# Optimization experiments

Measured on AMD Instinct MI355X. Metric: run time of the kernel, lower is better.

## Reference

```python
import math
import jax, jax.numpy as jnp
import numpy as np

C, NH, NL, NP, NLAYERS, FFN = 256, 8, 3, 4, 6, 1024
DH = C // NH
SHAPES = ((64, 64), (32, 32), (16, 16))  # (H,W) for res3, res4, res5
SIZES = [h * w for h, w in SHAPES]
STARTS = np.cumsum([0] + SIZES[:-1]).tolist()
EPS = 1e-5


def _sin_pe(H, W):
    d = C // 4
    y = jnp.arange(H, dtype=jnp.float32)[:, None]
    x = jnp.arange(W, dtype=jnp.float32)[None, :]
    div = jnp.exp(jnp.arange(d, dtype=jnp.float32) * (-math.log(10000.0) / d))[:, None, None]
    pe = jnp.concatenate([
        jnp.broadcast_to(jnp.sin(y * div), (d, H, W)),
        jnp.broadcast_to(jnp.cos(y * div), (d, H, W)),
        jnp.broadcast_to(jnp.sin(x * div), (d, H, W)),
        jnp.broadcast_to(jnp.cos(x * div), (d, H, W)),
    ], axis=0)  # (C,H,W)
    return pe.reshape(C, H * W).T  # (HW, C)


def _ref_points():
    pts = []
    for H, W in SHAPES:
        y = jnp.linspace(0.5 / H, 1.0 - 0.5 / H, H)
        x = jnp.linspace(0.5 / W, 1.0 - 0.5 / W, W)
        ry, rx = jnp.meshgrid(y, x, indexing='ij')
        pts.append(jnp.stack([rx.ravel(), ry.ravel()], -1))
    return jnp.concatenate(pts, 0)[None, :, None, :]  # (1,N,1,2), same per level


def _layernorm(x, g, b):
    mu = x.mean(-1, keepdims=True)
    v = ((x - mu) ** 2).mean(-1, keepdims=True)
    return (x - mu) * jax.lax.rsqrt(v + EPS) * g + b


def _bilinear(v, loc, H, W):
    # v: (B,HW,NH,DH); loc: (B,N,NH,NP,2) in [0,1]; grid_sample align_corners=False, zero pad
    B, N = loc.shape[0], loc.shape[1]
    x = loc[..., 0] * W - 0.5
    y = loc[..., 1] * H - 0.5
    x0 = jnp.floor(x); y0 = jnp.floor(y)
    wx = x - x0; wy = y - y0
    x0i = x0.astype(jnp.int32); y0i = y0.astype(jnp.int32)
    v_t = jnp.transpose(v, (0, 2, 1, 3))  # (B,NH,HW,DH)

    def corner(xi, yi, w):
        valid = (xi >= 0) & (xi < W) & (yi >= 0) & (yi < H)
        idx = jnp.clip(yi, 0, H - 1) * W + jnp.clip(xi, 0, W - 1)  # (B,N,NH,NP)
        idx = jnp.transpose(idx, (0, 2, 1, 3)).reshape(B, NH, N * NP)
        g = jnp.take_along_axis(v_t, idx[..., None], axis=2)  # (B,NH,N*NP,DH)
        g = g.reshape(B, NH, N, NP, DH).transpose(0, 2, 1, 3, 4)
        return g * (w * valid)[..., None]

    return (corner(x0i, y0i, (1 - wx) * (1 - wy))
            + corner(x0i + 1, y0i, wx * (1 - wy))
            + corner(x0i, y0i + 1, (1 - wx) * wy)
            + corner(x0i + 1, y0i + 1, wx * wy))


def _forward(res2, res3, res4, res5, level_embed, off_W, off_b, aw_W, aw_b, val_W, val_b,
             out_W, out_b, ln1_g, ln1_b, fc1_W, fc1_b, fc2_W, fc2_b, ln2_g, ln2_b,
             lat_W, lat_b, sm_W, sm_b, gn_g, gn_b):
    feats = [res3, res4, res5]
    B = res3.shape[0]
    flat = jnp.concatenate(
        [f.reshape(B, C, -1).transpose(0, 2, 1) + level_embed[i] for i, f in enumerate(feats)], 1)
    pe = jnp.concatenate([_sin_pe(H, W) for H, W in SHAPES], 0)[None]  # (1,N,C)
    ref = _ref_points()  # (1,N,1,2)
    normalizer = jnp.array([[W, H] for H, W in SHAPES], jnp.float32)  # (NL,2) as (W,H)
    N = flat.shape[1]

    x = flat
    for l in range(NLAYERS):
        q = x + pe
        value = (x @ val_W[l].T + val_b[l]).reshape(B, N, NH, DH)
        off = (q @ off_W[l].T + off_b[l]).reshape(B, N, NH, NL, NP, 2)
        aw = jax.nn.softmax((q @ aw_W[l].T + aw_b[l]).reshape(B, N, NH, NL * NP), -1)
        aw = aw.reshape(B, N, NH, NL, NP)
        loc = ref[:, :, None, :, None, :] + off / normalizer[None, None, None, :, None, :]
        attn = jnp.zeros((B, N, NH, DH), x.dtype)
        for li, (H, W) in enumerate(SHAPES):
            v_l = value[:, STARTS[li]:STARTS[li] + SIZES[li]]
            samp = _bilinear(v_l, loc[:, :, :, li], H, W)  # (B,N,NH,NP,DH)
            attn = attn + jnp.einsum('bnhpd,bnhp->bnhd', samp, aw[:, :, :, li])
        attn = attn.reshape(B, N, C) @ out_W[l].T + out_b[l]
        x = _layernorm(x + attn, ln1_g[l], ln1_b[l])
        h = jax.nn.relu(x @ fc1_W[l].T + fc1_b[l]) @ fc2_W[l].T + fc2_b[l]
        x = _layernorm(x + h, ln2_g[l], ln2_b[l])

    outs = []
    for li, (H, W) in enumerate(SHAPES):
        tok = x[:, STARTS[li]:STARTS[li] + SIZES[li]]
        outs.append(tok.transpose(0, 2, 1).reshape(B, C, H, W))
    o3, o4, o5 = outs

    r2_lat = jnp.einsum('bchw,oc->bohw', res2, lat_W) + lat_b[None, :, None, None]
    Hr, Wr = res2.shape[2], res2.shape[3]
    r3_up = jax.image.resize(o3, (B, C, Hr, Wr), method='bilinear')
    s = jax.lax.conv_general_dilated(r2_lat + r3_up, sm_W, (1, 1), ((1, 1), (1, 1)),
                                     dimension_numbers=('NCHW', 'OIHW', 'NCHW'))
    s = s + sm_b[None, :, None, None]
    # GroupNorm(32, C)
    g = s.reshape(B, 32, C // 32, Hr, Wr)
    mu = g.mean((2, 3, 4), keepdims=True)
    var = jnp.var(g, axis=(2, 3, 4), keepdims=True)
    g = (g - mu) * jax.lax.rsqrt(var + EPS)
    s = g.reshape(B, C, Hr, Wr) * gn_g[None, :, None, None] + gn_b[None, :, None, None]
    s = jax.nn.gelu(s, approximate=False)
    return s, o3, o4, o5


def setup_inputs() -> dict:
    key = jax.random.key(0)
    ks = jax.random.split(key, 16)
    def rn(k, shape, s=0.02):
        return jax.random.normal(k, shape, jnp.float32) * s
    B = 2
    L = NLAYERS
    return {
        'res2': jax.random.normal(ks[0], (B, C, 128, 128), jnp.float32),
        'res3': jax.random.normal(ks[1], (B, C, 64, 64), jnp.float32),
        'res4': jax.random.normal(ks[2], (B, C, 32, 32), jnp.float32),
        'res5': jax.random.normal(ks[3], (B, C, 16, 16), jnp.float32),
        'level_embed': rn(ks[4], (NL, C)),
        'off_W': rn(ks[5], (L, NH * NL * NP * 2, C)), 'off_b': jnp.zeros((L, NH * NL * NP * 2)),
        'aw_W': rn(ks[6], (L, NH * NL * NP, C)), 'aw_b': jnp.zeros((L, NH * NL * NP)),
        'val_W': rn(ks[7], (L, C, C)), 'val_b': jnp.zeros((L, C)),
        'out_W': rn(ks[8], (L, C, C)), 'out_b': jnp.zeros((L, C)),
        'ln1_g': jnp.ones((L, C)), 'ln1_b': jnp.zeros((L, C)),
        'fc1_W': rn(ks[9], (L, FFN, C)), 'fc1_b': jnp.zeros((L, FFN)),
        'fc2_W': rn(ks[10], (L, C, FFN)), 'fc2_b': jnp.zeros((L, C)),
        'ln2_g': jnp.ones((L, C)), 'ln2_b': jnp.zeros((L, C)),
        'lat_W': rn(ks[11], (C, C)), 'lat_b': jnp.zeros((C,)),
        'sm_W': rn(ks[12], (C, C, 3, 3)), 'sm_b': jnp.zeros((C,)),
        'gn_g': jnp.ones((C,)), 'gn_b': jnp.zeros((C,)),
    }


def reference(res2, res3, res4, res5, level_embed, off_W, off_b, aw_W, aw_b, val_W, val_b,
              out_W, out_b, ln1_g, ln1_b, fc1_W, fc1_b, fc2_W, fc2_b, ln2_g, ln2_b,
              lat_W, lat_b, sm_W, sm_b, gn_g, gn_b):
    return _forward(res2, res3, res4, res5, level_embed, off_W, off_b, aw_W, aw_b,
                    val_W, val_b, out_W, out_b, ln1_g, ln1_b, fc1_W, fc1_b, fc2_W, fc2_b,
                    ln2_g, ln2_b, lat_W, lat_b, sm_W, sm_b, gn_g, gn_b)
```

## Files before the change

### kernel.cpp

```cpp
#include <hip/hip_runtime.h>

namespace {
constexpr int Bn   = 2;
constexpr int Cc   = 256;
constexpr int Ntok = 5376;
constexpr int Ffn  = 1024;
constexpr int HW2  = 128 * 128;
constexpr float EPSf = 1e-5f;
constexpr int WL   = 729088;
}

typedef __attribute__((ext_vector_type(8))) short bf16x8;
typedef __attribute__((ext_vector_type(4))) float f32x4;

__device__ inline unsigned short f2bf(float x) {
  unsigned u = __float_as_uint(x);
  return (unsigned short)((u + 0x7fffu + ((u >> 16) & 1u)) >> 16);
}
__device__ inline float bf2f(unsigned short b) {
  return __uint_as_float((unsigned)b << 16);
}

__device__ inline void store_chunk_f32(unsigned short* lds, int row, int g,
                                       const float* v8) {
  int sg = g ^ (row & 7);
  unsigned short tmp[8];
#pragma unroll
  for (int j = 0; j < 8; j++) tmp[j] = f2bf(v8[j]);
  *reinterpret_cast<uint4*>(&lds[row * 64 + sg * 8]) =
      *reinterpret_cast<const uint4*>(tmp);
}
__device__ inline void store_chunk_bf(unsigned short* lds, int row, int g,
                                      uint4 v) {
  int sg = g ^ (row & 7);
  *reinterpret_cast<uint4*>(&lds[row * 64 + sg * 8]) = v;
}

__global__ __launch_bounds__(256) void wprep(
    const float* __restrict__ valW, const float* __restrict__ offW,
    const float* __restrict__ awW, const float* __restrict__ outW,
    const float* __restrict__ fc1W, const float* __restrict__ fc2W,
    const float* __restrict__ latW, const float* __restrict__ smW,
    unsigned short* __restrict__ wbf, unsigned short* __restrict__ wlat,
    unsigned short* __restrict__ wt) {
  int bx = blockIdx.x;
  int tid = threadIdx.x;
  if (bx < 4272) {
    int i4 = bx * 256 + tid;
    int l = i4 / 182272;
    int e = (i4 - l * 182272) * 4;
    const float* src;
    int off;
    if (e < 65536) { src = valW + (size_t)l * 65536; off = e; }
    else if (e < 139264) {
      int j = e - 65536;
      if (j < 49152) { src = offW + (size_t)l * 49152; off = j; }
      else { src = awW + (size_t)l * 24576; off = j - 49152; }
    } else if (e < 204800) { src = outW + (size_t)l * 65536; off = e - 139264; }
    else if (e < 466944) { src = fc1W + (size_t)l * 262144; off = e - 204800; }
    else { src = fc2W + (size_t)l * 262144; off = e - 466944; }
    float4 v = *reinterpret_cast<const float4*>(&src[off]);
    unsigned short t[4] = {f2bf(v.x), f2bf(v.y), f2bf(v.z), f2bf(v.w)};
    *reinterpret_cast<uint2*>(&wbf[(size_t)l * WL + e]) =
        *reinterpret_cast<const uint2*>(t);
  } else if (bx < 4336) {
    int e = ((bx - 4272) * 256 + tid) * 4;
    float4 v = *reinterpret_cast<const float4*>(&latW[e]);
    unsigned short t[4] = {f2bf(v.x), f2bf(v.y), f2bf(v.z), f2bf(v.w)};
    *reinterpret_cast<uint2*>(&wlat[e]) = *reinterpret_cast<const uint2*>(t);
  } else {
    int i = (bx - 4336) * 256 + tid;
    int o = i / 2304;
    int r = i - o * 2304;
    int tap = r >> 8;
    int c = r & 255;
    wt[i] = f2bf(smW[((size_t)(o * 256 + c)) * 9 + tap]);
  }
}

__global__ void flatten_kernel(const float* __restrict__ r3,
                               const float* __restrict__ r4,
                               const float* __restrict__ r5,
                               const float* __restrict__ lemb,
                               float* __restrict__ x,
                               unsigned short* __restrict__ xb,
                               unsigned short* __restrict__ qb,
                               unsigned short* __restrict__ peb) {
  const int NPC = Ntok * Cc;
  for (int i = blockIdx.x * blockDim.x + threadIdx.x; i < Bn * NPC;
       i += gridDim.x * blockDim.x) {
    int c = i & 255;
    int rest = i >> 8;
    int p = rest % Ntok;
    int b = rest / Ntok;
    int li = (p < 4096) ? 0 : ((p < 5120) ? 1 : 2);
    int start = (li == 0) ? 0 : ((li == 1) ? 4096 : 5120);
    int size = (li == 0) ? 4096 : ((li == 1) ? 1024 : 256);
    const float* f = (li == 0) ? r3 : ((li == 1) ? r4 : r5);
    int sp = p - start;
    int shift = 6 - li;
    int W = 64 >> li;
    int iy = sp >> shift;
    int ix = sp & (W - 1);
    int j = c & 63;
    int sel = c >> 6;
    float div = expf(-(float)j * (9.210340371976184f / 64.f));
    float coord = (sel < 2) ? (float)iy : (float)ix;
    float arg = coord * div;
    unsigned short pe16 = f2bf((sel & 1) ? cosf(arg) : sinf(arg));
    float v = f[((size_t)(b * Cc + c)) * size + sp] + lemb[li * Cc + c];
    x[i] = v;
    xb[i] = f2bf(v);
    qb[i] = f2bf(v + bf2f(pe16));
    peb[i - b * NPC] = pe16;
  }
}

template <int ACT, int OBF>
__global__ __launch_bounds__(256) void gemm_mfma_b(
    const unsigned short* __restrict__ A, const unsigned short* __restrict__ Wb,
    const float* __restrict__ bias, void* __restrict__ outp,
    int M, int N, int K, int nbx) {
  __shared__ unsigned short As[64 * 64];
  __shared__ unsigned short Ws[128 * 64];
  const int tid = threadIdx.x;
  const int nwg = gridDim.x;
  const int swz = (blockIdx.x & 7) * (nwg >> 3) + (blockIdx.x >> 3);
  const int m0 = (swz / nbx) * 64, n0 = (swz % nbx) * 128;
  const int wid = tid >> 6, lane = tid & 63;
  const int wm = wid >> 1, wn = wid & 1;
  const int lr = lane & 15, lh = lane >> 4;
  const int r8 = tid >> 3, g8 = tid & 7;
  f32x4 acc[2][4];
#pragma unroll
  for (int i = 0; i < 2; i++)
#pragma unroll
    for (int j = 0; j < 4; j++) acc[i][j] = f32x4{0.f, 0.f, 0.f, 0.f};

  uint4 ra[2], rw[4];
  const uint4 z4 = uint4{0, 0, 0, 0};
#pragma unroll
  for (int i = 0; i < 2; i++)
    ra[i] = *reinterpret_cast<const uint4*>(
        &A[(size_t)(m0 + r8 + i * 32) * K + g8 * 8]);
#pragma unroll
  for (int i = 0; i < 4; i++) {
    int n = n0 + r8 + i * 32;
    rw[i] = (n < N) ? *reinterpret_cast<const uint4*>(
                          &Wb[(size_t)n * K + g8 * 8])
                    : z4;
  }

  for (int k0 = 0; k0 < K; k0 += 64) {
    if (k0) __syncthreads();
#pragma unroll
    for (int i = 0; i < 2; i++) store_chunk_bf(As, r8 + i * 32, g8, ra[i]);
#pragma unroll
    for (int i = 0; i < 4; i++) store_chunk_bf(Ws, r8 + i * 32, g8, rw[i]);
    __syncthreads();
    int kn = k0 + 64;
    if (kn < K) {
#pragma unroll
      for (int i = 0; i < 2; i++)
        ra[i] = *reinterpret_cast<const uint4*>(
            &A[(size_t)(m0 + r8 + i * 32) * K + kn + g8 * 8]);
#pragma unroll
      for (int i = 0; i < 4; i++) {
        int n = n0 + r8 + i * 32;
        rw[i] = (n < N) ? *reinterpret_cast<const uint4*>(
                              &Wb[(size_t)n * K + kn + g8 * 8])
                        : z4;
      }
    }
    bf16x8 af[2][2], bfr[4][2];
#pragma unroll
    for (int mi = 0; mi < 2; mi++) {
      int r = wm * 32 + mi * 16 + lr;
#pragma unroll
      for (int s = 0; s < 2; s++) {
        int g = s * 4 + lh;
        af[mi][s] =
            *reinterpret_cast<const bf16x8*>(&As[r * 64 + (g ^ (r & 7)) * 8]);
      }
    }
#pragma unroll
    for (int nj = 0; nj < 4; nj++) {
      int r = wn * 64 + nj * 16 + lr;
#pragma unroll
      for (int s = 0; s < 2; s++) {
        int g = s * 4 + lh;
        bfr[nj][s] =
            *reinterpret_cast<const bf16x8*>(&Ws[r * 64 + (g ^ (r & 7)) * 8]);
      }
    }
#pragma unroll
    for (int mi = 0; mi < 2; mi++)
#pragma unroll
      for (int nj = 0; nj < 4; nj++) {
        acc[mi][nj] = __builtin_amdgcn_mfma_f32_16x16x32_bf16(
            af[mi][0], bfr[nj][0], acc[mi][nj], 0, 0, 0);
        acc[mi][nj] = __builtin_amdgcn_mfma_f32_16x16x32_bf16(
            af[mi][1], bfr[nj][1], acc[mi][nj], 0, 0, 0);
      }
  }
#pragma unroll
  for (int mi = 0; mi < 2; mi++) {
    int row = m0 + wm * 32 + mi * 16 + lh * 4;
#pragma unroll
    for (int nj = 0; nj < 4; nj++) {
      int col = n0 + wn * 64 + nj * 16 + lr;
      if (col >= N) continue;
      float b = bias[col];
#pragma unroll
      for (int r = 0; r < 4; r++) {
        float v = acc[mi][nj][r] + b;
        if (ACT) v = fmaxf(v, 0.f);
        if (OBF)
          ((unsigned short*)outp)[(size_t)(row + r) * N + col] = f2bf(v);
        else
          ((float*)outp)[(size_t)(row + r) * N + col] = v;
      }
    }
  }
}

template <int WRITEQ, int TOKOUT>
__global__ __launch_bounds__(256) void gemm_ln(
    const unsigned short* __restrict__ A, const unsigned short* __restrict__ Wb,
    const float* __restrict__ bias, const float* __restrict__ g,
    const float* __restrict__ bta, float* __restrict__ x,
    unsigned short* __restrict__ xb, const unsigned short* __restrict__ peb,
    unsigned short* __restrict__ qb, int K, float* __restrict__ o3,
    float* __restrict__ o4, float* __restrict__ o5) {
  __shared__ unsigned short As[32 * 64];
  __shared__ unsigned short Ws[256 * 64];
  __shared__ float pred[2][2][16];
  __shared__ float qred[2][2][16];
  const int tid = threadIdx.x;
  const int swz = (blockIdx.x & 7) * 42 + (blockIdx.x >> 3);
  const int m0 = swz * 32;
  const int wid = tid >> 6, lane = tid & 63;
  const int wm = wid >> 1, wn = wid & 1;
  const int lr = lane & 15, lh = lane >> 4;
  const int r8 = tid >> 3, g8 = tid & 7;
  f32x4 acc[8];
#pragma unroll
  for (int i = 0; i < 8; i++) acc[i] = f32x4{0.f, 0.f, 0.f, 0.f};

  uint4 ra, rw[8];
  ra = *reinterpret_cast<const uint4*>(&A[(size_t)(m0 + r8) * K + g8 * 8]);
#pragma unroll
  for (int i = 0; i < 8; i++)
    rw[i] = *reinterpret_cast<const uint4*>(
        &Wb[(size_t)(r8 + i * 32) * K + g8 * 8]);

  for (int k0 = 0; k0 < K; k0 += 64) {
    if (k0) __syncthreads();
    store_chunk_bf(As, r8, g8, ra);
#pragma unroll
    for (int i = 0; i < 8; i++) store_chunk_bf(Ws, r8 + i * 32, g8, rw[i]);
    __syncthreads();
    int kn = k0 + 64;
    if (kn < K) {
      ra = *reinterpret_cast<const uint4*>(
          &A[(size_t)(m0 + r8) * K + kn + g8 * 8]);
#pragma unroll
      for (int i = 0; i < 8; i++)
        rw[i] = *reinterpret_cast<const uint4*>(
            &Wb[(size_t)(r8 + i * 32) * K + kn + g8 * 8]);
    }
    bf16x8 af[2];
    {
      int r = wm * 16 + lr;
#pragma unroll
      for (int s = 0; s < 2; s++) {
        int gg2 = s * 4 + lh;
        af[s] =
            *reinterpret_cast<const bf16x8*>(&As[r * 64 + (gg2 ^ (r & 7)) * 8]);
      }
    }
#pragma unroll
    for (int nt = 0; nt < 8; nt++) {
      int r = wn * 128 + nt * 16 + lr;
      bf16x8 b0 =
          *reinterpret_cast<const bf16x8*>(&Ws[r * 64 + (lh ^ (r & 7)) * 8]);
      bf16x8 b1 = *reinterpret_cast<const bf16x8*>(
          &Ws[r * 64 + ((4 + lh) ^ (r & 7)) * 8]);
      acc[nt] =
          __builtin_amdgcn_mfma_f32_16x16x32_bf16(af[0], b0, acc[nt], 0, 0, 0);
      acc[nt] =
          __builtin_amdgcn_mfma_f32_16x16x32_bf16(af[1], b1, acc[nt], 0, 0, 0);
    }
  }

  const int rowl = wm * 16 + lh * 4;
#pragma unroll
  for (int nt = 0; nt < 8; nt++) {
    int col = wn * 128 + nt * 16 + lr;
    float bs = bias[col];
#pragma unroll
    for (int r = 0; r < 4; r++)
      acc[nt][r] += bs + x[(size_t)(m0 + rowl + r) * 256 + col];
  }
  float sum[4];
#pragma unroll
  for (int r = 0; r < 4; r++) {
    float s = 0.f;
#pragma unroll
    for (int nt = 0; nt < 8; nt++) s += acc[nt][r];
#pragma unroll
    for (int o = 8; o > 0; o >>= 1) s += __shfl_xor(s, o);
    sum[r] = s;
  }
  if (lr == 0) {
#pragma unroll
    for (int r = 0; r < 4; r++) pred[wm][wn][lh * 4 + r] = sum[r];
  }
  __syncthreads();
  float mu[4];
#pragma unroll
  for (int r = 0; r < 4; r++)
    mu[r] = (pred[wm][0][lh * 4 + r] + pred[wm][1][lh * 4 + r]) * (1.f / 256.f);
  float qs[4];
#pragma unroll
  for (int r = 0; r < 4; r++) {
    float q = 0.f;
#pragma unroll
    for (int nt = 0; nt < 8; nt++) {
      float d = acc[nt][r] - mu[r];
      q += d * d;
    }
#pragma unroll
    for (int o = 8; o > 0; o >>= 1) q += __shfl_xor(q, o);
    qs[r] = q;
  }
  if (lr == 0) {
#pragma unroll
    for (int r = 0; r < 4; r++) qred[wm][wn][lh * 4 + r] = qs[r];
  }
  __syncthreads();
  float rstd[4];
#pragma unroll
  for (int r = 0; r < 4; r++)
    rstd[r] = rsqrtf(
        (qred[wm][0][lh * 4 + r] + qred[wm][1][lh * 4 + r]) * (1.f / 256.f) +
        EPSf);
  float oarr[8][4];
#pragma unroll
  for (int nt = 0; nt < 8; nt++) {
    int col = wn * 128 + nt * 16 + lr;
    float gw = g[col], bw = bta[col];
#pragma unroll
    for (int r = 0; r < 4; r++) {
      int row = m0 + rowl + r;
      size_t idx = (size_t)row * 256 + col;
      float o = (acc[nt][r] - mu[r]) * rstd[r] * gw + bw;
      x[idx] = o;
      xb[idx] = f2bf(o);
      if (WRITEQ) {
        size_t pc = idx - (row >= Ntok ? (size_t)Ntok * 256 : 0);
        qb[idx] = f2bf(o + bf2f(peb[pc]));
      }
      if (TOKOUT) oarr[nt][r] = o;
    }
  }
  if constexpr (TOKOUT) {
    __shared__ float tout[32][129];
    int bb = (m0 >= Ntok) ? 1 : 0;
    int n = m0 - bb * Ntok;
    float* outp;
    int osize, ostart;
    if (n < 4096) { outp = o3; osize = 4096; ostart = 0; }
    else if (n < 5120) { outp = o4; osize = 1024; ostart = 4096; }
    else { outp = o5; osize = 256; ostart = 5120; }
    int sp0 = n - ostart;
#pragma unroll
    for (int hh = 0; hh < 2; hh++) {
      __syncthreads();
      if (wn == hh) {
#pragma unroll
        for (int nt = 0; nt < 8; nt++) {
          int cl = nt * 16 + lr;
#pragma unroll
          for (int r = 0; r < 4; r++) tout[rowl + r][cl] = oarr[nt][r];
        }
      }
      __syncthreads();
      int cl = tid & 127, rh = tid >> 7;
      float* dst =
          outp + ((size_t)(bb * 256 + hh * 128 + cl)) * osize + sp0 + rh * 16;
#pragma unroll
      for (int i = 0; i < 16; i += 4) {
        float4 v4 = {tout[rh * 16 + i + 0][cl], tout[rh * 16 + i + 1][cl],
                     tout[rh * 16 + i + 2][cl], tout[rh * 16 + i + 3][cl]};
        *reinterpret_cast<float4*>(&dst[i]) = v4;
      }
    }
  }
}

__global__ __launch_bounds__(256) void gemm_head(
    const unsigned short* __restrict__ xb, const unsigned short* __restrict__ qb,
    const unsigned short* __restrict__ wv, const unsigned short* __restrict__ wo,
    const float* __restrict__ valB, const float* __restrict__ offB,
    const float* __restrict__ awB, unsigned short* __restrict__ valO,
    float* __restrict__ offO, float* __restrict__ awO) {
  __shared__ unsigned short As[64 * 64];
  __shared__ unsigned short Ws[128 * 64];
  const int tid = threadIdx.x;
  const int swz = (blockIdx.x & 7) * 105 + (blockIdx.x >> 3);
  const bool isval = swz < 336;
  const unsigned short* A;
  const unsigned short* W;
  int m0, n0, Nn;
  if (isval) {
    A = xb; W = wv; Nn = 256;
    m0 = (swz >> 1) * 64; n0 = (swz & 1) * 128;
  } else {
    int s = swz - 336;
    A = qb; W = wo; Nn = 288;
    m0 = (s / 3) * 64; n0 = (s % 3) * 128;
  }
  const int wid = tid >> 6, lane = tid & 63;
  const int wm = wid >> 1, wn = wid & 1;
  const int lr = lane & 15, lh = lane >> 4;
  const int r8 = tid >> 3, g8 = tid & 7;
  f32x4 acc[2][4];
#pragma unroll
  for (int i = 0; i < 2; i++)
#pragma unroll
    for (int j = 0; j < 4; j++) acc[i][j] = f32x4{0.f, 0.f, 0.f, 0.f};

  uint4 ra[2], rw[4];
  const uint4 z4 = uint4{0, 0, 0, 0};
#pragma unroll
  for (int i = 0; i < 2; i++)
    ra[i] = *reinterpret_cast<const uint4*>(
        &A[(size_t)(m0 + r8 + i * 32) * 256 + g8 * 8]);
#pragma unroll
  for (int i = 0; i < 4; i++) {
    int n = n0 + r8 + i * 32;
    rw[i] = (n < Nn) ? *reinterpret_cast<const uint4*>(
                           &W[(size_t)n * 256 + g8 * 8])
                     : z4;
  }

  for (int k0 = 0; k0 < 256; k0 += 64) {
    if (k0) __syncthreads();
#pragma unroll
    for (int i = 0; i < 2; i++) store_chunk_bf(As, r8 + i * 32, g8, ra[i]);
#pragma unroll
    for (int i = 0; i < 4; i++) store_chunk_bf(Ws, r8 + i * 32, g8, rw[i]);
    __syncthreads();
    int kn = k0 + 64;
    if (kn < 256) {
#pragma unroll
      for (int i = 0; i < 2; i++)
        ra[i] = *reinterpret_cast<const uint4*>(
            &A[(size_t)(m0 + r8 + i * 32) * 256 + kn + g8 * 8]);
#pragma unroll
      for (int i = 0; i < 4; i++) {
        int n = n0 + r8 + i * 32;
        rw[i] = (n < Nn) ? *reinterpret_cast<const uint4*>(
                               &W[(size_t)n * 256 + kn + g8 * 8])
                         : z4;
      }
    }
    bf16x8 af[2][2], bfr[4][2];
#pragma unroll
    for (int mi = 0; mi < 2; mi++) {
      int r = wm * 32 + mi * 16 + lr;
#pragma unroll
      for (int s = 0; s < 2; s++) {
        int g = s * 4 + lh;
        af[mi][s] =
            *reinterpret_cast<const bf16x8*>(&As[r * 64 + (g ^ (r & 7)) * 8]);
      }
    }
#pragma unroll
    for (int nj = 0; nj < 4; nj++) {
      int r = wn * 64 + nj * 16 + lr;
#pragma unroll
      for (int s = 0; s < 2; s++) {
        int g = s * 4 + lh;
        bfr[nj][s] =
            *reinterpret_cast<const bf16x8*>(&Ws[r * 64 + (g ^ (r & 7)) * 8]);
      }
    }
#pragma unroll
    for (int mi = 0; mi < 2; mi++)
#pragma unroll
      for (int nj = 0; nj < 4; nj++) {
        acc[mi][nj] = __builtin_amdgcn_mfma_f32_16x16x32_bf16(
            af[mi][0], bfr[nj][0], acc[mi][nj], 0, 0, 0);
        acc[mi][nj] = __builtin_amdgcn_mfma_f32_16x16x32_bf16(
            af[mi][1], bfr[nj][1], acc[mi][nj], 0, 0, 0);
      }
  }
#pragma unroll
  for (int mi = 0; mi < 2; mi++) {
    int row = m0 + wm * 32 + mi * 16 + lh * 4;
#pragma unroll
    for (int nj = 0; nj < 4; nj++) {
      int col = n0 + wn * 64 + nj * 16 + lr;
      if (isval) {
        float b = valB[col];
#pragma unroll
        for (int r = 0; r < 4; r++)
          valO[(size_t)(row + r) * 256 + col] = f2bf(acc[mi][nj][r] + b);
      } else {
        if (col >= 288) continue;
        float b = (col < 192) ? offB[col] : awB[col - 192];
#pragma unroll
        for (int r = 0; r < 4; r++) {
          float v = acc[mi][nj][r] + b;
          if (col < 192)
            offO[(size_t)(row + r) * 192 + col] = v;
          else
            awO[(size_t)(row + r) * 96 + col - 192] = v;
        }
      }
    }
  }
}

__global__ __launch_bounds__(256) void msda_fused(
    const unsigned short* __restrict__ value, const float* __restrict__ off,
    const float* __restrict__ awl, unsigned short* __restrict__ attn) {
  __shared__ int recI[8][12][4];
  __shared__ float recW[8][12][4];
  const int tid = threadIdx.x;
  if (tid < 96) {
    int gq = tid / 12;
    int p = tid - gq * 12;
    int gid = blockIdx.x * 8 + gq;
    int h = gid & 7;
    int bn = gid >> 3;
    int n = bn % Ntok;
    int b = bn / Ntok;
    int li0 = (n < 4096) ? 0 : ((n < 5120) ? 1 : 2);
    int start0 = (li0 == 0) ? 0 : ((li0 == 1) ? 4096 : 5120);
    int shift = 6 - li0;
    int Wn = 1 << shift;
    int sp = n - start0;
    int iy = sp >> shift;
    int ix = sp & (Wn - 1);
    float refx = (ix + 0.5f) / (float)Wn;
    float refy = (iy + 0.5f) / (float)Wn;
    const float* ap = awl + (size_t)bn * 96 + h * 12;
    float lg[12];
    float mx = -1e30f;
#pragma unroll
    for (int j = 0; j < 12; j++) { lg[j] = ap[j]; mx = fmaxf(mx, lg[j]); }
    float ssum = 0.f;
#pragma unroll
    for (int j = 0; j < 12; j++) { lg[j] = expf(lg[j] - mx); ssum += lg[j]; }
    float w = lg[p] / ssum;
    int li = p >> 2;
    int HWl = 64 >> li;
    int st = (li == 0) ? 0 : ((li == 1) ? 4096 : 5120);
    const float* op = off + (size_t)bn * 192 + h * 24;
    float ox = op[p * 2 + 0];
    float oy = op[p * 2 + 1];
    float lx = refx + ox / (float)HWl;
    float ly = refy + oy / (float)HWl;
    float fx = lx * (float)HWl - 0.5f;
    float fy = ly * (float)HWl - 0.5f;
    float x0f = floorf(fx), y0f = floorf(fy);
    float wx = fx - x0f, wy = fy - y0f;
    int ix0 = (int)x0f, iy0 = (int)y0f;
    int base = (b * Ntok + st) * 256 + h * 32;
#pragma unroll
    for (int cr = 0; cr < 4; cr++) {
      int cx = ix0 + (cr & 1);
      int cy = iy0 + (cr >> 1);
      bool valid = (cx >= 0) & (cx < HWl) & (cy >= 0) & (cy < HWl);
      float wc = ((cr & 1) ? wx : 1.f - wx) * ((cr >> 1) ? wy : 1.f - wy);
      int cxc = min(max(cx, 0), HWl - 1);
      int cyc = min(max(cy, 0), HWl - 1);
      recI[gq][p][cr] = base + (cyc * HWl + cxc) * 256;
      recW[gq][p][cr] = valid ? (w * wc) : 0.f;
    }
  }
  __syncthreads();
  const int grp = tid >> 5, lane = tid & 31;
  const unsigned short* vb = value + lane;
  float acc = 0.f;
#pragma unroll
  for (int p = 0; p < 12; p++) {
    int4 idx = *reinterpret_cast<const int4*>(&recI[grp][p][0]);
    float4 w = *reinterpret_cast<const float4*>(&recW[grp][p][0]);
    acc += w.x * bf2f(vb[idx.x]);
    acc += w.y * bf2f(vb[idx.y]);
    acc += w.z * bf2f(vb[idx.z]);
    acc += w.w * bf2f(vb[idx.w]);
  }
  int gid = blockIdx.x * 8 + grp;
  attn[(size_t)gid * 32 + lane] = f2bf(acc);
}

__global__ __launch_bounds__(256) void conv3x3_mfma(
    const unsigned short* __restrict__ T, const unsigned short* __restrict__ Wt,
    const float* __restrict__ bias, unsigned short* __restrict__ out) {
  __shared__ unsigned short As[64 * 64];
  __shared__ unsigned short Ws[128 * 64];
  const int tid = threadIdx.x;
  const int nwg = gridDim.x;
  const int swz = (blockIdx.x & 7) * (nwg >> 3) + (blockIdx.x >> 3);
  const int m0 = (swz >> 1) * 64, n0 = (swz & 1) * 128;
  const int b = m0 >> 14;
  const int p0 = m0 & 16383;
  const int y = p0 >> 7;
  const int x0 = p0 & 127;
  const int wid = tid >> 6, lane = tid & 63;
  const int wm = wid >> 1, wn = wid & 1;
  const int lr = lane & 15, lh = lane >> 4;
  const int r8 = tid >> 3, g8 = tid & 7;
  f32x4 acc[2][4];
#pragma unroll
  for (int i = 0; i < 2; i++)
#pragma unroll
    for (int j = 0; j < 4; j++) acc[i][j] = f32x4{0.f, 0.f, 0.f, 0.f};

  uint4 ra[2], rw[4];
  auto loadA = [&](int kc, uint4* r) {
    int tap = kc >> 2;
    int cb = (kc & 3) * 64;
    int dy = tap / 3 - 1, dx = tap % 3 - 1;
    int yy = y + dy;
#pragma unroll
    for (int i = 0; i < 2; i++) {
      int row = r8 + i * 32;
      int xx = x0 + row + dx;
      uint4 v = uint4{0, 0, 0, 0};
      if (yy >= 0 && yy < 128 && xx >= 0 && xx < 128)
        v = *reinterpret_cast<const uint4*>(
            &T[((size_t)(b * 16384 + yy * 128 + xx)) * 256 + cb + g8 * 8]);
      r[i] = v;
    }
  };
  auto loadW = [&](int kc, uint4* r) {
#pragma unroll
    for (int i = 0; i < 4; i++)
      r[i] = *reinterpret_cast<const uint4*>(
          &Wt[(size_t)(n0 + r8 + i * 32) * 2304 + kc * 64 + g8 * 8]);
  };
  loadA(0, ra);
  loadW(0, rw);

  for (int kc = 0; kc < 36; kc++) {
    if (kc) __syncthreads();
#pragma unroll
    for (int i = 0; i < 2; i++) store_chunk_bf(As, r8 + i * 32, g8, ra[i]);
#pragma unroll
    for (int i = 0; i < 4; i++) store_chunk_bf(Ws, r8 + i * 32, g8, rw[i]);
    __syncthreads();
    if (kc + 1 < 36) {
      loadA(kc + 1, ra);
      loadW(kc + 1, rw);
    }
    bf16x8 af[2][2], bfr[4][2];
#pragma unroll
    for (int mi = 0; mi < 2; mi++) {
      int r = wm * 32 + mi * 16 + lr;
#pragma unroll
      for (int s = 0; s < 2; s++) {
        int g = s * 4 + lh;
        af[mi][s] =
            *reinterpret_cast<const bf16x8*>(&As[r * 64 + (g ^ (r & 7)) * 8]);
      }
    }
#pragma unroll
    for (int nj = 0; nj < 4; nj++) {
      int r = wn * 64 + nj * 16 + lr;
#pragma unroll
      for (int s = 0; s < 2; s++) {
        int g = s * 4 + lh;
        bfr[nj][s] =
            *reinterpret_cast<const bf16x8*>(&Ws[r * 64 + (g ^ (r & 7)) * 8]);
      }
    }
#pragma unroll
    for (int mi = 0; mi < 2; mi++)
#pragma unroll
      for (int nj = 0; nj < 4; nj++) {
        acc[mi][nj] = __builtin_amdgcn_mfma_f32_16x16x32_bf16(
            af[mi][0], bfr[nj][0], acc[mi][nj], 0, 0, 0);
        acc[mi][nj] = __builtin_amdgcn_mfma_f32_16x16x32_bf16(
            af[mi][1], bfr[nj][1], acc[mi][nj], 0, 0, 0);
      }
  }
#pragma unroll
  for (int mi = 0; mi < 2; mi++) {
    int row = m0 + wm * 32 + mi * 16 + lh * 4;
#pragma unroll
    for (int nj = 0; nj < 4; nj++) {
      int col = n0 + wn * 64 + nj * 16 + lr;
      float b = bias[col];
#pragma unroll
      for (int r = 0; r < 4; r++)
        out[(size_t)(row + r) * 256 + col] = f2bf(acc[mi][nj][r] + b);
    }
  }
}

__global__ __launch_bounds__(256) void gemm_tn_mfma(
    const float* __restrict__ A, const unsigned short* __restrict__ Wb,
    const float* __restrict__ bias, const float* __restrict__ x,
    unsigned short* __restrict__ out) {
  __shared__ unsigned short As[64 * 64];
  __shared__ unsigned short Ws[128 * 64];
  const int tid = threadIdx.x;
  const int nwg = gridDim.x;
  const int swz = (blockIdx.x & 7) * (nwg >> 3) + (blockIdx.x >> 3);
  const int m0 = (swz >> 1) * 64, n0 = (swz & 1) * 128;
  const int b = m0 >> 14;
  const int p0 = m0 & 16383;
  const int wid = tid >> 6, lane = tid & 63;
  const int wm = wid >> 1, wn = wid & 1;
  const int lr = lane & 15, lh = lane >> 4;
  const int r8 = tid >> 3, g8 = tid & 7;
  const int arow = tid & 63, agb = tid >> 6;
  f32x4 acc[2][4];
#pragma unroll
  for (int i = 0; i < 2; i++)
#pragma unroll
    for (int j = 0; j < 4; j++) acc[i][j] = f32x4{0.f, 0.f, 0.f, 0.f};

  float va[16];
  uint4 rw[4];
  auto loadA = [&](int k0, float* v) {
#pragma unroll
    for (int i = 0; i < 2; i++) {
      int g = agb + i * 4;
#pragma unroll
      for (int j = 0; j < 8; j++)
        v[i * 8 + j] =
            A[(size_t)(b * 256 + k0 + g * 8 + j) * 16384 + p0 + arow];
    }
  };
  auto loadW = [&](int k0, uint4* r) {
#pragma unroll
    for (int i = 0; i < 4; i++)
      r[i] = *reinterpret_cast<const uint4*>(
          &Wb[(size_t)(n0 + r8 + i * 32) * 256 + k0 + g8 * 8]);
  };
  loadA(0, va);
  loadW(0, rw);

  for (int k0 = 0; k0 < 256; k0 += 64) {
    if (k0) __syncthreads();
#pragma unroll
    for (int i = 0; i < 2; i++)
      store_chunk_f32(As, arow, agb + i * 4, &va[i * 8]);
#pragma unroll
    for (int i = 0; i < 4; i++) store_chunk_bf(Ws, r8 + i * 32, g8, rw[i]);
    __syncthreads();
    int kn = k0 + 64;
    if (kn < 256) {
      loadA(kn, va);
      loadW(kn, rw);
    }
    bf16x8 af[2][2], bfr[4][2];
#pragma unroll
    for (int mi = 0; mi < 2; mi++) {
      int r = wm * 32 + mi * 16 + lr;
#pragma unroll
      for (int s = 0; s < 2; s++) {
        int g = s * 4 + lh;
        af[mi][s] =
            *reinterpret_cast<const bf16x8*>(&As[r * 64 + (g ^ (r & 7)) * 8]);
      }
    }
#pragma unroll
    for (int nj = 0; nj < 4; nj++) {
      int r = wn * 64 + nj * 16 + lr;
#pragma unroll
      for (int s = 0; s < 2; s++) {
        int g = s * 4 + lh;
        bfr[nj][s] =
            *reinterpret_cast<const bf16x8*>(&Ws[r * 64 + (g ^ (r & 7)) * 8]);
      }
    }
#pragma unroll
    for (int mi = 0; mi < 2; mi++)
#pragma unroll
      for (int nj = 0; nj < 4; nj++) {
        acc[mi][nj] = __builtin_amdgcn_mfma_f32_16x16x32_bf16(
            af[mi][0], bfr[nj][0], acc[mi][nj], 0, 0, 0);
        acc[mi][nj] = __builtin_amdgcn_mfma_f32_16x16x32_bf16(
            af[mi][1], bfr[nj][1], acc[mi][nj], 0, 0, 0);
      }
  }
  const float* xbse = x + (size_t)b * Ntok * 256;
#pragma unroll
  for (int mi = 0; mi < 2; mi++) {
    int row0 = m0 + wm * 32 + mi * 16 + lh * 4;
#pragma unroll
    for (int r = 0; r < 4; r++) {
      int p = (row0 + r) & 16383;
      int Y = p >> 7, X = p & 127;
      float yc = Y * 0.5f - 0.25f;
      float y0f = floorf(yc);
      float wy = yc - y0f;
      int y0 = (int)y0f;
      int y0c = min(max(y0, 0), 63), y1c = min(max(y0 + 1, 0), 63);
      float xc = X * 0.5f - 0.25f;
      float x0f = floorf(xc);
      float wx = xc - x0f;
      int xq0 = (int)x0f;
      int x0c = min(max(xq0, 0), 63), x1c = min(max(xq0 + 1, 0), 63);
      const float* r00 = xbse + (size_t)(y0c * 64 + x0c) * 256;
      const float* r01 = xbse + (size_t)(y0c * 64 + x1c) * 256;
      const float* r10 = xbse + (size_t)(y1c * 64 + x0c) * 256;
      const float* r11 = xbse + (size_t)(y1c * 64 + x1c) * 256;
#pragma unroll
      for (int nj = 0; nj < 4; nj++) {
        int col = n0 + wn * 64 + nj * 16 + lr;
        float up = (1.f - wy) * ((1.f - wx) * r00[col] + wx * r01[col]) +
                   wy * ((1.f - wx) * r10[col] + wx * r11[col]);
        out[(size_t)(row0 + r) * 256 + col] =
            f2bf(acc[mi][nj][r] + bias[col] + up);
      }
    }
  }
}

__global__ __launch_bounds__(256) void gn_partial(
    const unsigned short* __restrict__ s, float* __restrict__ part) {
  int blk = blockIdx.x;
  int pr = blk & 15;
  int bg = blk >> 4;
  int g = bg & 31;
  int b = bg >> 5;
  int tid = threadIdx.x;
  float sum = 0.f, sq = 0.f;
  for (int e = pr * 8192 + tid; e < (pr + 1) * 8192; e += 256) {
    int p = e >> 3, cc = e & 7;
    float v = bf2f(s[((size_t)(b * 16384 + p)) * 256 + g * 8 + cc]);
    sum += v;
    sq += v * v;
  }
  __shared__ float rs[256], rq[256];
  rs[tid] = sum;
  rq[tid] = sq;
  __syncthreads();
  for (int st = 128; st > 0; st >>= 1) {
    if (tid < st) { rs[tid] += rs[tid + st]; rq[tid] += rq[tid + st]; }
    __syncthreads();
  }
  if (tid == 0) {
    part[(size_t)blk * 2 + 0] = rs[0];
    part[(size_t)blk * 2 + 1] = rq[0];
  }
}

__global__ void gn_final(const float* __restrict__ part,
                         float* __restrict__ stats) {
  int tid = threadIdx.x;
  if (tid < 64) {
    float s = 0.f, q = 0.f;
    for (int j = 0; j < 16; j++) {
      s += part[(size_t)(tid * 16 + j) * 2 + 0];
      q += part[(size_t)(tid * 16 + j) * 2 + 1];
    }
    float mu = s * (1.f / 131072.f);
    float var = q * (1.f / 131072.f) - mu * mu;
    stats[tid * 2 + 0] = mu;
    stats[tid * 2 + 1] = rsqrtf(var + EPSf);
  }
}

__global__ void gn_apply(const unsigned short* __restrict__ s,
                         const float* __restrict__ stats,
                         const float* __restrict__ gg,
                         const float* __restrict__ gb,
                         float* __restrict__ out) {
  __shared__ float tile[32][33];
  int p0 = blockIdx.x * 32, c0 = blockIdx.y * 32, b = blockIdx.z;
  int tx = threadIdx.x, tyy = threadIdx.y;
  int c = c0 + tx;
  float mu = stats[(b * 32 + (c >> 3)) * 2 + 0];
  float rstd = stats[(b * 32 + (c >> 3)) * 2 + 1];
  float gw = gg[c], bw = gb[c];
  for (int i = tyy; i < 32; i += 8) {
    float v = bf2f(s[((size_t)(b * 16384 + p0 + i)) * 256 + c]);
    v = (v - mu) * rstd * gw + bw;
    v = 0.5f * v * (1.f + erff(v * 0.70710678118654752f));
    tile[i][tx] = v;
  }
  __syncthreads();
  for (int i = tyy; i < 32; i += 8)
    out[((size_t)(b * 256 + c0 + i)) * 16384 + p0 + tx] = tile[tx][i];
}

extern "C" void kernel_launch(void* const* d_in, const int* in_sizes, int n_in,
                              void* d_out, int out_size, void* d_ws,
                              size_t ws_size, hipStream_t stream) {
  (void)in_sizes; (void)n_in; (void)out_size; (void)ws_size;
  const float* res2  = (const float*)d_in[0];
  const float* res3  = (const float*)d_in[1];
  const float* res4  = (const float*)d_in[2];
  const float* res5  = (const float*)d_in[3];
  const float* lemb  = (const float*)d_in[4];
  const float* off_W = (const float*)d_in[5];
  const float* off_b = (const float*)d_in[6];
  const float* aw_W  = (const float*)d_in[7];
  const float* aw_b  = (const float*)d_in[8];
  const float* val_W = (const float*)d_in[9];
  const float* val_b = (const float*)d_in[10];
  const float* out_W = (const float*)d_in[11];
  const float* out_b = (const float*)d_in[12];
  const float* ln1_g = (const float*)d_in[13];
  const float* ln1_b = (const float*)d_in[14];
  const float* fc1_W = (const float*)d_in[15];
  const float* fc1_b = (const float*)d_in[16];
  const float* fc2_W = (const float*)d_in[17];
  const float* fc2_b = (const float*)d_in[18];
  const float* ln2_g = (const float*)d_in[19];
  const float* ln2_b = (const float*)d_in[20];
  const float* lat_W = (const float*)d_in[21];
  const float* lat_b = (const float*)d_in[22];
  const float* sm_W  = (const float*)d_in[23];
  const float* sm_b  = (const float*)d_in[24];
  const float* gn_g  = (const float*)d_in[25];
  const float* gn_b  = (const float*)d_in[26];

  float* ws = (float*)d_ws;
  float*          x      = ws;
  unsigned short* xb     = (unsigned short*)(ws + 2752512);
  unsigned short* peb    = (unsigned short*)(ws + 4128768);
  unsigned short* qb     = (unsigned short*)(ws + 4816896);
  unsigned short* valueb = (unsigned short*)(ws + 6193152);
  float*          offb   = ws + 7569408;
  float*          awl    = ws + 9633792;
  unsigned short* attnb  = (unsigned short*)(ws + 10665984);
  unsigned short* hb     = (unsigned short*)(ws + 14794752);
  unsigned short* tbuf   = hb;
  unsigned short* wtbuf  = (unsigned short*)(ws + 20299776);
  float*          gnpart = ws + 20594688;
  float*          gnstat = ws + 20596736;
  unsigned short* wbf    = (unsigned short*)(ws + 20596864);
  unsigned short* wlat   = wbf + (size_t)6 * WL;
  unsigned short* sbufb  = (unsigned short*)ws;

  float* out_s  = (float*)d_out;
  float* out_o3 = out_s + (size_t)Bn * Cc * HW2;
  float* out_o4 = out_o3 + (size_t)Bn * Cc * 4096;
  float* out_o5 = out_o4 + (size_t)Bn * Cc * 1024;

  const int M = Bn * Ntok;

  flatten_kernel<<<1024, 256, 0, stream>>>(res3, res4, res5, lemb, x, xb, qb,
                                           peb);
  wprep<<<6640, 256, 0, stream>>>(val_W, off_W, aw_W, out_W, fc1_W, fc2_W,
                                  lat_W, sm_W, wbf, wlat, wtbuf);

  for (int l = 0; l < 6; l++) {
    const unsigned short* wl = wbf + (size_t)l * WL;
    gemm_head<<<840, 256, 0, stream>>>(
        xb, qb, wl + 0, wl + 65536, val_b + l * 256, off_b + l * 192,
        aw_b + l * 96, valueb, offb, awl);
    msda_fused<<<10752, 256, 0, stream>>>(valueb, offb, awl, attnb);
    gemm_ln<0, 0><<<336, 256, 0, stream>>>(
        attnb, wl + 139264, out_b + l * 256, ln1_g + l * 256, ln1_b + l * 256,
        x, xb, peb, qb, 256, nullptr, nullptr, nullptr);
    gemm_mfma_b<1, 1><<<1344, 256, 0, stream>>>(
        xb, wl + 204800, fc1_b + l * 1024, hb, M, 1024, 256, 8);
    if (l < 5)
      gemm_ln<1, 0><<<336, 256, 0, stream>>>(
          hb, wl + 466944, fc2_b + l * 256, ln2_g + l * 256, ln2_b + l * 256,
          x, xb, peb, qb, 1024, nullptr, nullptr, nullptr);
    else
      gemm_ln<0, 1><<<336, 256, 0, stream>>>(
          hb, wl + 466944, fc2_b + l * 256, ln2_g + l * 256, ln2_b + l * 256,
          x, xb, peb, qb, 1024, out_o3, out_o4, out_o5);
  }

  gemm_tn_mfma<<<1024, 256, 0, stream>>>(res2, wlat, lat_b, x, tbuf);
  conv3x3_mfma<<<1024, 256, 0, stream>>>(tbuf, wtbuf, sm_b, sbufb);
  gn_partial<<<1024, 256, 0, stream>>>(sbufb, gnpart);
  gn_final<<<1, 64, 0, stream>>>(gnpart, gnstat);
  gn_apply<<<dim3(512, 8, 2), dim3(32, 8), 0, stream>>>(sbufb, gnstat, gn_g,
                                                        gn_b, out_s);
}
```

Before: 739.1 us.

## Merge setup kernels, halve gemm_head M-tile, parallelize MSDA softmax

Folds the flatten and weight-prep kernels into one setup launch, removing one launch and letting the two independent jobs share the GPU. Cuts gemm_head's M tile from 64 to 32 rows and doubles its grid, giving more workgroups to spread across CUs at the cost of reusing each weight tile less. In msda_fused, each of the 12 sampling threads now computes only its own exp and shares it through LDS, instead of every thread exponentiating all 12 logits. That softmax change adds an extra barrier.

```diff
diff --git a/kernel.cpp b/kernel.cpp
--- a/kernel.cpp
+++ b/kernel.cpp
@@ -36,7 +36,11 @@
   *reinterpret_cast<uint4*>(&lds[row * 64 + sg * 8]) = v;
 }
 
-__global__ __launch_bounds__(256) void wprep(
+__global__ __launch_bounds__(256) void setup_all(
+    const float* __restrict__ r3, const float* __restrict__ r4,
+    const float* __restrict__ r5, const float* __restrict__ lemb,
+    float* __restrict__ x, unsigned short* __restrict__ xb,
+    unsigned short* __restrict__ qb, unsigned short* __restrict__ peb,
     const float* __restrict__ valW, const float* __restrict__ offW,
     const float* __restrict__ awW, const float* __restrict__ outW,
     const float* __restrict__ fc1W, const float* __restrict__ fc2W,
@@ -45,8 +49,39 @@
     unsigned short* __restrict__ wt) {
   int bx = blockIdx.x;
   int tid = threadIdx.x;
-  if (bx < 4272) {
-    int i4 = bx * 256 + tid;
+  if (bx < 1024) {
+    const int NPC = Ntok * Cc;
+    for (int i = bx * 256 + tid; i < Bn * NPC; i += 1024 * 256) {
+      int c = i & 255;
+      int rest = i >> 8;
+      int p = rest % Ntok;
+      int b = rest / Ntok;
+      int li = (p < 4096) ? 0 : ((p < 5120) ? 1 : 2);
+      int start = (li == 0) ? 0 : ((li == 1) ? 4096 : 5120);
+      int size = (li == 0) ? 4096 : ((li == 1) ? 1024 : 256);
+      const float* f = (li == 0) ? r3 : ((li == 1) ? r4 : r5);
+      int sp = p - start;
+      int shift = 6 - li;
+      int W = 64 >> li;
+      int iy = sp >> shift;
+      int ix = sp & (W - 1);
+      int j = c & 63;
+      int sel = c >> 6;
+      float div = expf(-(float)j * (9.210340371976184f / 64.f));
+      float coord = (sel < 2) ? (float)iy : (float)ix;
+      float arg = coord * div;
+      unsigned short pe16 = f2bf((sel & 1) ? cosf(arg) : sinf(arg));
+      float v = f[((size_t)(b * Cc + c)) * size + sp] + lemb[li * Cc + c];
+      x[i] = v;
+      xb[i] = f2bf(v);
+      qb[i] = f2bf(v + bf2f(pe16));
+      peb[i - b * NPC] = pe16;
+    }
+    return;
+  }
+  int b2 = bx - 1024;
+  if (b2 < 4272) {
+    int i4 = b2 * 256 + tid;
     int l = i4 / 182272;
     int e = (i4 - l * 182272) * 4;
     const float* src;
@@ -63,56 +98,18 @@
     unsigned short t[4] = {f2bf(v.x), f2bf(v.y), f2bf(v.z), f2bf(v.w)};
     *reinterpret_cast<uint2*>(&wbf[(size_t)l * WL + e]) =
         *reinterpret_cast<const uint2*>(t);
-  } else if (bx < 4336) {
-    int e = ((bx - 4272) * 256 + tid) * 4;
+  } else if (b2 < 4336) {
+    int e = ((b2 - 4272) * 256 + tid) * 4;
     float4 v = *reinterpret_cast<const float4*>(&latW[e]);
     unsigned short t[4] = {f2bf(v.x), f2bf(v.y), f2bf(v.z), f2bf(v.w)};
     *reinterpret_cast<uint2*>(&wlat[e]) = *reinterpret_cast<const uint2*>(t);
   } else {
-    int i = (bx - 4336) * 256 + tid;
+    int i = (b2 - 4336) * 256 + tid;
     int o = i / 2304;
     int r = i - o * 2304;
     int tap = r >> 8;
     int c = r & 255;
     wt[i] = f2bf(smW[((size_t)(o * 256 + c)) * 9 + tap]);
-  }
-}
-
-__global__ void flatten_kernel(const float* __restrict__ r3,
-                               const float* __restrict__ r4,
-                               const float* __restrict__ r5,
-                               const float* __restrict__ lemb,
-                               float* __restrict__ x,
-                               unsigned short* __restrict__ xb,
-                               unsigned short* __restrict__ qb,
-                               unsigned short* __restrict__ peb) {
-  const int NPC = Ntok * Cc;
-  for (int i = blockIdx.x * blockDim.x + threadIdx.x; i < Bn * NPC;
-       i += gridDim.x * blockDim.x) {
-    int c = i & 255;
-    int rest = i >> 8;
-    int p = rest % Ntok;
-    int b = rest / Ntok;
-    int li = (p < 4096) ? 0 : ((p < 5120) ? 1 : 2);
-    int start = (li == 0) ? 0 : ((li == 1) ? 4096 : 5120);
-    int size = (li == 0) ? 4096 : ((li == 1) ? 1024 : 256);
-    const float* f = (li == 0) ? r3 : ((li == 1) ? r4 : r5);
-    int sp = p - start;
-    int shift = 6 - li;
-    int W = 64 >> li;
-    int iy = sp >> shift;
-    int ix = sp & (W - 1);
-    int j = c & 63;
-    int sel = c >> 6;
-    float div = expf(-(float)j * (9.210340371976184f / 64.f));
-    float coord = (sel < 2) ? (float)iy : (float)ix;
-    float arg = coord * div;
-    unsigned short pe16 = f2bf((sel & 1) ? cosf(arg) : sinf(arg));
-    float v = f[((size_t)(b * Cc + c)) * size + sp] + lemb[li * Cc + c];
-    x[i] = v;
-    xb[i] = f2bf(v);
-    qb[i] = f2bf(v + bf2f(pe16));
-    peb[i - b * NPC] = pe16;
   }
 }
 
@@ -405,38 +402,33 @@
     const float* __restrict__ valB, const float* __restrict__ offB,
     const float* __restrict__ awB, unsigned short* __restrict__ valO,
     float* __restrict__ offO, float* __restrict__ awO) {
-  __shared__ unsigned short As[64 * 64];
+  __shared__ unsigned short As[32 * 64];
   __shared__ unsigned short Ws[128 * 64];
   const int tid = threadIdx.x;
-  const int swz = (blockIdx.x & 7) * 105 + (blockIdx.x >> 3);
-  const bool isval = swz < 336;
+  const int swz = (blockIdx.x & 7) * 210 + (blockIdx.x >> 3);
+  const bool isval = swz < 672;
   const unsigned short* A;
   const unsigned short* W;
   int m0, n0, Nn;
   if (isval) {
     A = xb; W = wv; Nn = 256;
-    m0 = (swz >> 1) * 64; n0 = (swz & 1) * 128;
+    m0 = (swz >> 1) * 32; n0 = (swz & 1) * 128;
   } else {
-    int s = swz - 336;
+    int s = swz - 672;
     A = qb; W = wo; Nn = 288;
-    m0 = (s / 3) * 64; n0 = (s % 3) * 128;
+    m0 = (s / 3) * 32; n0 = (s % 3) * 128;
   }
   const int wid = tid >> 6, lane = tid & 63;
   const int wm = wid >> 1, wn = wid & 1;
   const int lr = lane & 15, lh = lane >> 4;
   const int r8 = tid >> 3, g8 = tid & 7;
-  f32x4 acc[2][4];
-#pragma unroll
-  for (int i = 0; i < 2; i++)
-#pragma unroll
-    for (int j = 0; j < 4; j++) acc[i][j] = f32x4{0.f, 0.f, 0.f, 0.f};
-
-  uint4 ra[2], rw[4];
+  f32x4 acc[4];
+#pragma unroll
+  for (int j = 0; j < 4; j++) acc[j] = f32x4{0.f, 0.f, 0.f, 0.f};
+
+  uint4 ra, rw[4];
   const uint4 z4 = uint4{0, 0, 0, 0};
-#pragma unroll
-  for (int i = 0; i < 2; i++)
-    ra[i] = *reinterpret_cast<const uint4*>(
-        &A[(size_t)(m0 + r8 + i * 32) * 256 + g8 * 8]);
+  ra = *reinterpret_cast<const uint4*>(&A[(size_t)(m0 + r8) * 256 + g8 * 8]);
 #pragma unroll
   for (int i = 0; i < 4; i++) {
     int n = n0 + r8 + i * 32;
@@ -447,17 +439,14 @@
 
   for (int k0 = 0; k0 < 256; k0 += 64) {
     if (k0) __syncthreads();
-#pragma unroll
-    for (int i = 0; i < 2; i++) store_chunk_bf(As, r8 + i * 32, g8, ra[i]);
+    store_chunk_bf(As, r8, g8, ra);
 #pragma unroll
     for (int i = 0; i < 4; i++) store_chunk_bf(Ws, r8 + i * 32, g8, rw[i]);
     __syncthreads();
     int kn = k0 + 64;
     if (kn < 256) {
-#pragma unroll
-      for (int i = 0; i < 2; i++)
-        ra[i] = *reinterpret_cast<const uint4*>(
-            &A[(size_t)(m0 + r8 + i * 32) * 256 + kn + g8 * 8]);
+      ra = *reinterpret_cast<const uint4*>(
+          &A[(size_t)(m0 + r8) * 256 + kn + g8 * 8]);
 #pragma unroll
       for (int i = 0; i < 4; i++) {
         int n = n0 + r8 + i * 32;
@@ -466,59 +455,48 @@
                          : z4;
       }
     }
-    bf16x8 af[2][2], bfr[4][2];
-#pragma unroll
-    for (int mi = 0; mi < 2; mi++) {
-      int r = wm * 32 + mi * 16 + lr;
+    bf16x8 af[2];
+    {
+      int r = wm * 16 + lr;
 #pragma unroll
       for (int s = 0; s < 2; s++) {
-        int g = s * 4 + lh;
-        af[mi][s] =
-            *reinterpret_cast<const bf16x8*>(&As[r * 64 + (g ^ (r & 7)) * 8]);
+        int gg2 = s * 4 + lh;
+        af[s] =
+            *reinterpret_cast<const bf16x8*>(&As[r * 64 + (gg2 ^ (r & 7)) * 8]);
       }
     }
 #pragma unroll
     for (int nj = 0; nj < 4; nj++) {
       int r = wn * 64 + nj * 16 + lr;
-#pragma unroll
-      for (int s = 0; s < 2; s++) {
-        int g = s * 4 + lh;
-        bfr[nj][s] =
-            *reinterpret_cast<const bf16x8*>(&Ws[r * 64 + (g ^ (r & 7)) * 8]);
-      }
-    }
-#pragma unroll
-    for (int mi = 0; mi < 2; mi++)
-#pragma unroll
-      for (int nj = 0; nj < 4; nj++) {
-        acc[mi][nj] = __builtin_amdgcn_mfma_f32_16x16x32_bf16(
-            af[mi][0], bfr[nj][0], acc[mi][nj], 0, 0, 0);
-        acc[mi][nj] = __builtin_amdgcn_mfma_f32_16x16x32_bf16(
-            af[mi][1], bfr[nj][1], acc[mi][nj], 0, 0, 0);
-      }
-  }
-#pragma unroll
-  for (int mi = 0; mi < 2; mi++) {
-    int row = m0 + wm * 32 + mi * 16 + lh * 4;
-#pragma unroll
-    for (int nj = 0; nj < 4; nj++) {
-      int col = n0 + wn * 64 + nj * 16 + lr;
-      if (isval) {
-        float b = valB[col];
-#pragma unroll
-        for (int r = 0; r < 4; r++)
-          valO[(size_t)(row + r) * 256 + col] = f2bf(acc[mi][nj][r] + b);
-      } else {
-        if (col >= 288) continue;
-        float b = (col < 192) ? offB[col] : awB[col - 192];
-#pragma unroll
-        for (int r = 0; r < 4; r++) {
-          float v = acc[mi][nj][r] + b;
-          if (col < 192)
-            offO[(size_t)(row + r) * 192 + col] = v;
-          else
-            awO[(size_t)(row + r) * 96 + col - 192] = v;
-        }
+      bf16x8 b0 =
+          *reinterpret_cast<const bf16x8*>(&Ws[r * 64 + (lh ^ (r & 7)) * 8]);
+      bf16x8 b1 = *reinterpret_cast<const bf16x8*>(
+          &Ws[r * 64 + ((4 + lh) ^ (r & 7)) * 8]);
+      acc[nj] =
+          __builtin_amdgcn_mfma_f32_16x16x32_bf16(af[0], b0, acc[nj], 0, 0, 0);
+      acc[nj] =
+          __builtin_amdgcn_mfma_f32_16x16x32_bf16(af[1], b1, acc[nj], 0, 0, 0);
+    }
+  }
+  const int row0 = m0 + wm * 16 + lh * 4;
+#pragma unroll
+  for (int nj = 0; nj < 4; nj++) {
+    int col = n0 + wn * 64 + nj * 16 + lr;
+    if (isval) {
+      float b = valB[col];
+#pragma unroll
+      for (int r = 0; r < 4; r++)
+        valO[(size_t)(row0 + r) * 256 + col] = f2bf(acc[nj][r] + b);
+    } else {
+      if (col >= 288) continue;
+      float b = (col < 192) ? offB[col] : awB[col - 192];
+#pragma unroll
+      for (int r = 0; r < 4; r++) {
+        float v = acc[nj][r] + b;
+        if (col < 192)
+          offO[(size_t)(row0 + r) * 192 + col] = v;
+        else
+          awO[(size_t)(row0 + r) * 96 + col - 192] = v;
       }
     }
   }
@@ -529,10 +507,15 @@
     const float* __restrict__ awl, unsigned short* __restrict__ attn) {
   __shared__ int recI[8][12][4];
   __shared__ float recW[8][12][4];
+  __shared__ float els[8][12];
   const int tid = threadIdx.x;
+  float e = 0.f;
+  int idxr[4];
+  float wcr[4];
+  int gq = 0, p = 0;
   if (tid < 96) {
-    int gq = tid / 12;
-    int p = tid - gq * 12;
+    gq = tid / 12;
+    p = tid - gq * 12;
     int gid = blockIdx.x * 8 + gq;
     int h = gid & 7;
     int bn = gid >> 3;
@@ -552,10 +535,8 @@
     float mx = -1e30f;
 #pragma unroll
     for (int j = 0; j < 12; j++) { lg[j] = ap[j]; mx = fmaxf(mx, lg[j]); }
-    float ssum = 0.f;
-#pragma unroll
-    for (int j = 0; j < 12; j++) { lg[j] = expf(lg[j] - mx); ssum += lg[j]; }
-    float w = lg[p] / ssum;
+    e = expf(lg[p] - mx);
+    els[gq][p] = e;
     int li = p >> 2;
     int HWl = 64 >> li;
     int st = (li == 0) ? 0 : ((li == 1) ? 4096 : 5120);
@@ -578,8 +559,20 @@
       float wc = ((cr & 1) ? wx : 1.f - wx) * ((cr >> 1) ? wy : 1.f - wy);
       int cxc = min(max(cx, 0), HWl - 1);
       int cyc = min(max(cy, 0), HWl - 1);
-      recI[gq][p][cr] = base + (cyc * HWl + cxc) * 256;
-      recW[gq][p][cr] = valid ? (w * wc) : 0.f;
+      idxr[cr] = base + (cyc * HWl + cxc) * 256;
+      wcr[cr] = valid ? wc : 0.f;
+    }
+  }
+  __syncthreads();
+  if (tid < 96) {
+    float ssum = 0.f;
+#pragma unroll
+    for (int j = 0; j < 12; j++) ssum += els[gq][j];
+    float w = e / ssum;
+#pragma unroll
+    for (int cr = 0; cr < 4; cr++) {
+      recI[gq][p][cr] = idxr[cr];
+      recW[gq][p][cr] = w * wcr[cr];
     }
   }
   __syncthreads();
@@ -587,9 +580,9 @@
   const unsigned short* vb = value + lane;
   float acc = 0.f;
 #pragma unroll
-  for (int p = 0; p < 12; p++) {
-    int4 idx = *reinterpret_cast<const int4*>(&recI[grp][p][0]);
-    float4 w = *reinterpret_cast<const float4*>(&recW[grp][p][0]);
+  for (int pp = 0; pp < 12; pp++) {
+    int4 idx = *reinterpret_cast<const int4*>(&recI[grp][pp][0]);
+    float4 w = *reinterpret_cast<const float4*>(&recW[grp][pp][0]);
     acc += w.x * bf2f(vb[idx.x]);
     acc += w.y * bf2f(vb[idx.y]);
     acc += w.z * bf2f(vb[idx.z]);
@@ -951,14 +944,13 @@
 
   const int M = Bn * Ntok;
 
-  flatten_kernel<<<1024, 256, 0, stream>>>(res3, res4, res5, lemb, x, xb, qb,
-                                           peb);
-  wprep<<<6640, 256, 0, stream>>>(val_W, off_W, aw_W, out_W, fc1_W, fc2_W,
-                                  lat_W, sm_W, wbf, wlat, wtbuf);
+  setup_all<<<7664, 256, 0, stream>>>(res3, res4, res5, lemb, x, xb, qb, peb,
+                                      val_W, off_W, aw_W, out_W, fc1_W, fc2_W,
+                                      lat_W, sm_W, wbf, wlat, wtbuf);
 
   for (int l = 0; l < 6; l++) {
     const unsigned short* wl = wbf + (size_t)l * WL;
-    gemm_head<<<840, 256, 0, stream>>>(
+    gemm_head<<<1680, 256, 0, stream>>>(
         xb, qb, wl + 0, wl + 65536, val_b + l * 256, off_b + l * 192,
         aw_b + l * 96, valueb, offb, awl);
     msda_fused<<<10752, 256, 0, stream>>>(valueb, offb, awl, attnb);
```

After: 718.7 us. -2.8%, faster.
